# Performance work log

Hardware: AMD Instinct MI355X
Metric: run time of the kernel (lower is better)

## Reference

```python
import jax, jax.numpy as jnp
import numpy as np
from jax import lax

TAU = 10.0
THR = 1.0
ALPHA = float(np.exp(-1.0 / TAU))  # leak factor exp(-dt/tau), dt=1


def conv2d(x, w, pad):
    # x: [N,C,H,W], w: [O,I,kh,kw]
    return lax.conv_general_dilated(
        x, w, window_strides=(1, 1), padding=[(pad, pad), (pad, pad)],
        dimension_numbers=('NCHW', 'OIHW', 'NCHW'))


def avgpool(x, k):
    n, c, h, w = x.shape
    return x.reshape(n, c, h // k, k, w // k, k).mean(axis=(3, 5))


def exp_leak(x):
    # x: [T, ...]; v[t] = alpha*v[t-1] + x[t]; outputs membrane each step
    def step(v, xt):
        v = ALPHA * v + xt
        return v, v
    _, y = lax.scan(step, jnp.zeros_like(x[0]), x)
    return y


def lif(x):
    # LIF with SingleSpike + MembraneSubtract reset (norm_input=False)
    def step(v, xt):
        v = ALPHA * v + xt
        s = (v >= THR).astype(v.dtype)
        return v - s * THR, s
    _, s = lax.scan(step, jnp.zeros_like(x[0]), x)
    return s


def forward(x, conv1_w, conv2_w, lin_w):
    B, T = x.shape[:2]
    h = avgpool(conv2d(x.reshape(B * T, 2, 32, 32), conv1_w, 2), 4)  # [BT,4,8,8]
    h = h.reshape(B, T, 4, 8, 8).swapaxes(0, 1)                       # [T,B,4,8,8]
    h = lif(exp_leak(h)).swapaxes(0, 1).reshape(B * T, 4, 8, 8)
    h = avgpool(conv2d(h, conv2_w, 1), 2)                             # [BT,8,4,4]
    h = h.reshape(B, T, 8, 4, 4).swapaxes(0, 1)                       # [T,B,8,4,4]
    h = lif(exp_leak(h)).swapaxes(0, 1).reshape(B, T, 8 * 4 * 4)      # [B,T,128]
    return jnp.einsum('btf,of->bto', h, lin_w)                        # [B,T,2]


def setup_inputs() -> dict:
    key = jax.random.key(0)
    k1, k2, k3, k4 = jax.random.split(key, 4)
    B, T = 128, 100
    x = jax.random.uniform(k1, (B, T, 2, 32, 32), dtype=jnp.float32)
    conv1_w = jax.random.normal(k2, (4, 2, 5, 5), dtype=jnp.float32) / np.sqrt(2 * 5 * 5)
    conv2_w = jax.random.normal(k3, (8, 4, 3, 3), dtype=jnp.float32) / np.sqrt(4 * 3 * 3)
    lin_w = jax.random.normal(k4, (2, 128), dtype=jnp.float32) / np.sqrt(128)
    return {'x': x, 'conv1_w': conv1_w, 'conv2_w': conv2_w, 'lin_w': lin_w}


def reference(x, conv1_w, conv2_w, lin_w):
    return forward(x, conv1_w, conv2_w, lin_w)
```

## Files before the change

### kernel.cpp

```cpp
#include <hip/hip_runtime.h>

#define ALPHA 0.90483741803595957f

__global__ void prep_weights(const float* __restrict__ w1, const float* __restrict__ w2,
                             float* __restrict__ w1e, float* __restrict__ w2e) {
    int idx = blockIdx.x * 256 + threadIdx.x;
    if (idx < 512) {
        int v = idx & 7, u = (idx >> 3) & 7, ch = (idx >> 6) & 1, oc = idx >> 7;
        float s = 0.f;
        for (int a = 0; a < 5; ++a) {
            int i = u - a; if (i < 0 || i > 3) continue;
            for (int b = 0; b < 5; ++b) {
                int j = v - b; if (j < 0 || j > 3) continue;
                s += w1[((oc * 2 + ch) * 5 + a) * 5 + b];
            }
        }
        w1e[idx] = s * (1.f / 16.f);
    } else if (idx < 1024) {
        int k = idx - 512;
        int v = k & 3, u = (k >> 2) & 3, ch = (k >> 4) & 3, oc = k >> 6;
        float s = 0.f;
        for (int a = 0; a < 3; ++a) {
            int i = u - a; if (i < 0 || i > 1) continue;
            for (int b = 0; b < 3; ++b) {
                int j = v - b; if (j < 0 || j > 1) continue;
                s += w2[((oc * 4 + ch) * 3 + a) * 3 + b];
            }
        }
        w2e[k] = s * 0.25f;
    }
}

__global__ __launch_bounds__(256) void conv1_pool(const float* __restrict__ x,
                                                  const float* __restrict__ w1e,
                                                  float* __restrict__ y1) {
    __shared__ __align__(16) float tile[4][2][36][36];
    int tid = threadIdx.x;

    float4* t4 = (float4*)&tile[0][0][0][0];
    #pragma unroll
    for (int k = 0; k < 11; ++k) {
        int i = tid + k * 256;
        if (i < 2592) t4[i] = make_float4(0.f, 0.f, 0.f, 0.f);
    }
    __syncthreads();

    int li = tid >> 6, pos = tid & 63;
    long gi = (long)blockIdx.x * 4 + li;
    const float* src = x + gi * 2048;
    #pragma unroll
    for (int k = 0; k < 8; ++k) {
        int e = k * 256 + pos * 4;
        float4 d = *(const float4*)(src + e);
        int ch = e >> 10, rem = e & 1023, r = rem >> 5, c = rem & 31;
        float* dst = &tile[li][ch][r + 2][c + 2];
        dst[0] = d.x; dst[1] = d.y; dst[2] = d.z; dst[3] = d.w;
    }
    __syncthreads();

    int p = pos >> 3, q = pos & 7;
    float acc0 = 0.f, acc1 = 0.f, acc2 = 0.f, acc3 = 0.f;
    #pragma unroll
    for (int ch = 0; ch < 2; ++ch) {
        #pragma unroll
        for (int r = 0; r < 8; ++r) {
            const float* row = &tile[li][ch][4 * p + r][4 * q];
            float4 a = *(const float4*)row;
            float4 b = *(const float4*)(row + 4);
            float in[8] = {a.x, a.y, a.z, a.w, b.x, b.y, b.z, b.w};
            #pragma unroll
            for (int c = 0; c < 8; ++c) {
                float xi = in[c];
                acc0 += w1e[((0 * 2 + ch) * 8 + r) * 8 + c] * xi;
                acc1 += w1e[((1 * 2 + ch) * 8 + r) * 8 + c] * xi;
                acc2 += w1e[((2 * 2 + ch) * 8 + r) * 8 + c] * xi;
                acc3 += w1e[((3 * 2 + ch) * 8 + r) * 8 + c] * xi;
            }
        }
    }
    float* dst = y1 + gi * 256 + pos;
    dst[0] = acc0; dst[64] = acc1; dst[128] = acc2; dst[192] = acc3;
}

#define READW(base, Q)                                                        \
    {                                                                         \
        _Pragma("unroll")                                                     \
        for (int rr = 0; rr < 4; ++rr) {                                      \
            _Pragma("unroll")                                                 \
            for (int cc = 0; cc < 4; ++cc) {                                  \
                float4 tq = *(const float4*)((base) + rr * 40 + cc * 4);      \
                int o = (rr * 4 + cc) * 4;                                    \
                Q[o + 0] = tq.x; Q[o + 1] = tq.y;                             \
                Q[o + 2] = tq.z; Q[o + 3] = tq.w;                             \
            }                                                                 \
        }                                                                     \
    }

#define SCAN1_WRITE(in0, in1, in2, in3, d0, d1)                               \
    {                                                                         \
        v10 = ALPHA * v10 + (in0); v20 = ALPHA * v20 + v10;                   \
        float s0 = (v20 >= 1.f) ? 1.f : 0.f; v20 -= s0;                       \
        v11 = ALPHA * v11 + (in1); v21 = ALPHA * v21 + v11;                   \
        float s1 = (v21 >= 1.f) ? 1.f : 0.f; v21 -= s1;                       \
        v12 = ALPHA * v12 + (in2); v22 = ALPHA * v22 + v12;                   \
        float s2 = (v22 >= 1.f) ? 1.f : 0.f; v22 -= s2;                       \
        v13 = ALPHA * v13 + (in3); v23 = ALPHA * v23 + v13;                   \
        float s3 = (v23 >= 1.f) ? 1.f : 0.f; v23 -= s3;                       \
        float4 sp = make_float4(s0, s1, s2, s3);                              \
        *(float4*)(d0) = sp;                                                  \
        *(float4*)(d1) = sp;                                                  \
    }

#define CONV_SCAN2_STORE(Q, t)                                                \
    {                                                                         \
        float acca = 0.f;                                                     \
        _Pragma("unroll")                                                     \
        for (int ch = 0; ch < 4; ++ch) {                                      \
            _Pragma("unroll")                                                 \
            for (int rr = 0; rr < 4; ++rr) {                                  \
                _Pragma("unroll")                                             \
                for (int cc = 0; cc < 4; ++cc) {                              \
                    acca += wa[ch * 16 + rr * 4 + cc] *                       \
                            Q[(rr * 4 + cc) * 4 + ch];                        \
                }                                                             \
            }                                                                 \
        }                                                                     \
        w1a = ALPHA * w1a + acca; w2a = ALPHA * w2a + w1a;                    \
        float sa = (w2a >= 1.f) ? 1.f : 0.f; w2a -= sa;                       \
        dst[(t) * 128] = sa;                                                  \
    }

__global__ __launch_bounds__(64, 1) void fused_wave(const float* __restrict__ y1,
                                                    const float* __restrict__ w2e,
                                                    float* __restrict__ s2g) {
    __shared__ float tE[808];
    __shared__ float tO[808];
    int lane = threadIdx.x;
    int b = blockIdx.x >> 1;
    int h = blockIdx.x & 1;

    #pragma unroll
    for (int k = 0; k < 13; ++k) {
        int i = lane + k * 64;
        if (i < 808) { tE[i] = 0.f; tO[i] = 0.f; }
    }

    int r1 = lane >> 3, c1 = lane & 7;
    int posq = ((r1 + 1) * 10 + (c1 + 1)) * 4;
    float* wE0 = &tE[posq];
    float* wE1 = &tE[404 + posq];
    float* wO0 = &tO[posq];
    float* wO1 = &tO[404 + posq];

    int oc = h * 4 + (lane >> 4), p = (lane >> 2) & 3, q = lane & 3;

    float wa[64];
    #pragma unroll
    for (int k = 0; k < 16; ++k) {
        float4 ta = *(const float4*)(w2e + oc * 64 + k * 4);
        wa[k * 4 + 0] = ta.x; wa[k * 4 + 1] = ta.y;
        wa[k * 4 + 2] = ta.z; wa[k * 4 + 3] = ta.w;
    }

    int rbq = ((2 * p) * 10 + 2 * q) * 4 + ((p & 1) ? 404 : 0);
    const float* rbE = &tE[rbq];
    const float* rbO = &tO[rbq];

    #pragma unroll
    for (int k = 0; k < 64; ++k) {
        asm volatile("" : "+v"(wa[k]));
    }

    const float* src = y1 + (long)b * 25600 + lane;
    float* dst = s2g + (long)b * 12800 + h * 64 + lane;

    float x0  = src[0],    x1  = src[64],   x2  = src[128],  x3  = src[192];
    float c10 = src[256],  c11 = src[320],  c12 = src[384],  c13 = src[448];
    float c20 = src[512],  c21 = src[576],  c22 = src[640],  c23 = src[704];
    float p10 = src[768],  p11 = src[832],  p12 = src[896],  p13 = src[960];
    float p20 = src[1024], p21 = src[1088], p22 = src[1152], p23 = src[1216];

    float v10 = 0.f, v20 = 0.f, v11 = 0.f, v21 = 0.f;
    float v12 = 0.f, v22 = 0.f, v13 = 0.f, v23 = 0.f;
    float w1a = 0.f, w2a = 0.f;

    float qa[64], qb[64];

    SCAN1_WRITE(x0, x1, x2, x3, wE0, wE1)
    READW(rbE, qa)

    for (int i = 0; i < 49; ++i) {
        int t5 = 2 * i + 5, t6 = 2 * i + 6;
        const float* a5 = src + (t5 < 100 ? t5 * 256 : 0);
        const float* a6 = src + (t6 < 100 ? t6 * 256 : 0);
        float n10 = a5[0], n11 = a5[64], n12 = a5[128], n13 = a5[192];
        float n20 = a6[0], n21 = a6[64], n22 = a6[128], n23 = a6[192];

        SCAN1_WRITE(c10, c11, c12, c13, wO0, wO1)
        READW(rbO, qb)
        CONV_SCAN2_STORE(qa, 2 * i)
        SCAN1_WRITE(c20, c21, c22, c23, wE0, wE1)
        READW(rbE, qa)
        CONV_SCAN2_STORE(qb, 2 * i + 1)

        c10 = p10; c11 = p11; c12 = p12; c13 = p13;
        c20 = p20; c21 = p21; c22 = p22; c23 = p23;
        p10 = n10; p11 = n11; p12 = n12; p13 = n13;
        p20 = n20; p21 = n21; p22 = n22; p23 = n23;
    }

    SCAN1_WRITE(c10, c11, c12, c13, wO0, wO1)
    READW(rbO, qb)
    CONV_SCAN2_STORE(qa, 98)
    CONV_SCAN2_STORE(qb, 99)
}

__global__ __launch_bounds__(256) void linear_out(const float* __restrict__ s2,
                                                  const float* __restrict__ lw,
                                                  float* __restrict__ out) {
    int tid = threadIdx.x;
    long bt = (long)blockIdx.x * 4 + (tid >> 6);
    int lane = tid & 63;
    float2 v = *(const float2*)(s2 + bt * 128 + lane * 2);
    float w00 = lw[lane * 2], w01 = lw[lane * 2 + 1];
    float w10 = lw[128 + lane * 2], w11 = lw[128 + lane * 2 + 1];
    float a0 = v.x * w00 + v.y * w01;
    float a1 = v.x * w10 + v.y * w11;
    #pragma unroll
    for (int off = 32; off; off >>= 1) {
        a0 += __shfl_down(a0, off);
        a1 += __shfl_down(a1, off);
    }
    if (lane == 0) { out[bt * 2] = a0; out[bt * 2 + 1] = a1; }
}

extern "C" void kernel_launch(void* const* d_in, const int* in_sizes, int n_in,
                              void* d_out, int out_size, void* d_ws, size_t ws_size,
                              hipStream_t stream) {
    const float* x  = (const float*)d_in[0];
    const float* w1 = (const float*)d_in[1];
    const float* w2 = (const float*)d_in[2];
    const float* lw = (const float*)d_in[3];
    float* out = (float*)d_out;

    float* ws   = (float*)d_ws;
    float* w1e  = ws;
    float* w2e  = ws + 512;
    float* y1   = ws + 1024;
    float* s2g  = y1 + 3276800;

    prep_weights<<<4, 256, 0, stream>>>(w1, w2, w1e, w2e);
    conv1_pool<<<3200, 256, 0, stream>>>(x, w1e, y1);
    fused_wave<<<256, 64, 0, stream>>>(y1, w2e, s2g);
    linear_out<<<3200, 256, 0, stream>>>(s2g, lw, out);
}
```

Measured before the change: 215.5 us.

## Stage per-batch conv1 output in LDS and merge channel halves into one block

The fused scan/conv2 kernel now runs one 128-thread block per batch element, with both 64-lane halves in the same block, instead of two separate 64-thread blocks. Before the sequential time loop, the block bulk-copies the whole 100 KB y1 slice for its batch into shared memory with float4 loads. Per-timestep global loads in the serial loop become LDS reads. This removes global latency from the critical path and halves the duplicate y1 reads, at the cost of large LDS use and a serialized upfront copy before compute starts.

Result: faster. 210.1 us (-2.5%).

```diff
diff --git a/kernel.cpp b/kernel.cpp
--- a/kernel.cpp
+++ b/kernel.cpp
@@ -130,27 +130,40 @@
         dst[(t) * 128] = sa;                                                  \
     }
 
-__global__ __launch_bounds__(64, 1) void fused_wave(const float* __restrict__ y1,
-                                                    const float* __restrict__ w2e,
-                                                    float* __restrict__ s2g) {
-    __shared__ float tE[808];
-    __shared__ float tO[808];
-    int lane = threadIdx.x;
-    int b = blockIdx.x >> 1;
-    int h = blockIdx.x & 1;
-
+#define LY(t, k) lds_y[(t) * 256 + (k) * 64 + lane]
+
+__global__ __launch_bounds__(128, 1) void fused_wave(const float* __restrict__ y1,
+                                                     const float* __restrict__ w2e,
+                                                     float* __restrict__ s2g) {
+    __shared__ float lds_y[25600];
+    __shared__ float tE[2][808];
+    __shared__ float tO[2][808];
+    int tid = threadIdx.x;
+    int lane = tid & 63;
+    int h = tid >> 6;
+    int b = blockIdx.x;
+
+    {
+        const float* gsrc = y1 + (long)b * 25600;
+        #pragma unroll 10
+        for (int k = 0; k < 50; ++k) {
+            int e = (k * 128 + tid) * 4;
+            *(float4*)(&lds_y[e]) = *(const float4*)(gsrc + e);
+        }
+    }
     #pragma unroll
     for (int k = 0; k < 13; ++k) {
         int i = lane + k * 64;
-        if (i < 808) { tE[i] = 0.f; tO[i] = 0.f; }
-    }
+        if (i < 808) { tE[h][i] = 0.f; tO[h][i] = 0.f; }
+    }
+    __syncthreads();
 
     int r1 = lane >> 3, c1 = lane & 7;
     int posq = ((r1 + 1) * 10 + (c1 + 1)) * 4;
-    float* wE0 = &tE[posq];
-    float* wE1 = &tE[404 + posq];
-    float* wO0 = &tO[posq];
-    float* wO1 = &tO[404 + posq];
+    float* wE0 = &tE[h][posq];
+    float* wE1 = &tE[h][404 + posq];
+    float* wO0 = &tO[h][posq];
+    float* wO1 = &tO[h][404 + posq];
 
     int oc = h * 4 + (lane >> 4), p = (lane >> 2) & 3, q = lane & 3;
 
@@ -161,24 +174,22 @@
         wa[k * 4 + 0] = ta.x; wa[k * 4 + 1] = ta.y;
         wa[k * 4 + 2] = ta.z; wa[k * 4 + 3] = ta.w;
     }
-
-    int rbq = ((2 * p) * 10 + 2 * q) * 4 + ((p & 1) ? 404 : 0);
-    const float* rbE = &tE[rbq];
-    const float* rbO = &tO[rbq];
-
     #pragma unroll
     for (int k = 0; k < 64; ++k) {
         asm volatile("" : "+v"(wa[k]));
     }
 
-    const float* src = y1 + (long)b * 25600 + lane;
+    int rbq = ((2 * p) * 10 + 2 * q) * 4 + ((p & 1) ? 404 : 0);
+    const float* rbE = &tE[h][rbq];
+    const float* rbO = &tO[h][rbq];
+
     float* dst = s2g + (long)b * 12800 + h * 64 + lane;
 
-    float x0  = src[0],    x1  = src[64],   x2  = src[128],  x3  = src[192];
-    float c10 = src[256],  c11 = src[320],  c12 = src[384],  c13 = src[448];
-    float c20 = src[512],  c21 = src[576],  c22 = src[640],  c23 = src[704];
-    float p10 = src[768],  p11 = src[832],  p12 = src[896],  p13 = src[960];
-    float p20 = src[1024], p21 = src[1088], p22 = src[1152], p23 = src[1216];
+    float x0  = LY(0, 0), x1  = LY(0, 1), x2  = LY(0, 2), x3  = LY(0, 3);
+    float c10 = LY(1, 0), c11 = LY(1, 1), c12 = LY(1, 2), c13 = LY(1, 3);
+    float c20 = LY(2, 0), c21 = LY(2, 1), c22 = LY(2, 2), c23 = LY(2, 3);
+    float p10 = LY(3, 0), p11 = LY(3, 1), p12 = LY(3, 2), p13 = LY(3, 3);
+    float p20 = LY(4, 0), p21 = LY(4, 1), p22 = LY(4, 2), p23 = LY(4, 3);
 
     float v10 = 0.f, v20 = 0.f, v11 = 0.f, v21 = 0.f;
     float v12 = 0.f, v22 = 0.f, v13 = 0.f, v23 = 0.f;
@@ -191,10 +202,9 @@
 
     for (int i = 0; i < 49; ++i) {
         int t5 = 2 * i + 5, t6 = 2 * i + 6;
-        const float* a5 = src + (t5 < 100 ? t5 * 256 : 0);
-        const float* a6 = src + (t6 < 100 ? t6 * 256 : 0);
-        float n10 = a5[0], n11 = a5[64], n12 = a5[128], n13 = a5[192];
-        float n20 = a6[0], n21 = a6[64], n22 = a6[128], n23 = a6[192];
+        int o5 = (t5 < 100 ? t5 : 0), o6 = (t6 < 100 ? t6 : 0);
+        float n10 = LY(o5, 0), n11 = LY(o5, 1), n12 = LY(o5, 2), n13 = LY(o5, 3);
+        float n20 = LY(o6, 0), n21 = LY(o6, 1), n22 = LY(o6, 2), n23 = LY(o6, 3);
 
         SCAN1_WRITE(c10, c11, c12, c13, wO0, wO1)
         READW(rbO, qb)
@@ -251,6 +261,6 @@
 
     prep_weights<<<4, 256, 0, stream>>>(w1, w2, w1e, w2e);
     conv1_pool<<<3200, 256, 0, stream>>>(x, w1e, y1);
-    fused_wave<<<256, 64, 0, stream>>>(y1, w2e, s2g);
+    fused_wave<<<128, 128, 0, stream>>>(y1, w2e, s2g);
     linear_out<<<3200, 256, 0, stream>>>(s2g, lw, out);
 }
```
